# Kernel tuning notes

Hardware: AMD Instinct MI355X
Metric: run time of the kernel (lower is better)

Reference implementation:

```python
import jax, jax.numpy as jnp
import numpy as np

NUM_USERS = 60000
NUM_ITEMS = 40000
NUM_NODES = NUM_USERS + NUM_ITEMS
EMB = 64
HID = 32
N_EDGES = 1600000
BATCH = 16384


def setup_inputs() -> dict:
    key = jax.random.key(0)
    ks = jax.random.split(key, 16)
    def xavier(k, shape):
        fan_in, fan_out = shape[1], shape[0]
        lim = float(np.sqrt(6.0 / (fan_in + fan_out)))
        return jax.random.uniform(k, shape, jnp.float32, -lim, lim)
    return {
        "user_ids": jax.random.randint(ks[0], (BATCH,), 0, NUM_USERS),
        "item_ids": jax.random.randint(ks[1], (BATCH,), 0, NUM_ITEMS),
        "adj_rows": jax.random.randint(ks[2], (N_EDGES,), 0, NUM_NODES),
        "adj_cols": jax.random.randint(ks[3], (N_EDGES,), 0, NUM_NODES),
        "adj_vals": jax.random.uniform(ks[4], (N_EDGES,), jnp.float32),
        # embeddings (xavier_uniform, matching init_weights)
        "user_emb_w": xavier(ks[5], (NUM_USERS, EMB)),
        "item_emb_w": xavier(ks[6], (NUM_ITEMS, EMB)),
        # GC layer 1: 64 -> 32 ; GC layer 2: 32 -> 64
        "gc1_w": xavier(ks[7], (HID, EMB)),
        "gc1_b": jnp.zeros((HID,), jnp.float32),
        "gc2_w": xavier(ks[8], (EMB, HID)),
        "gc2_b": jnp.zeros((EMB,), jnp.float32),
        # predictor: Linear(2*EMB -> HID), ReLU, Linear(HID -> 1), Sigmoid
        "p1_w": xavier(ks[9], (HID, 2 * EMB)),
        "p1_b": jnp.zeros((HID,), jnp.float32),
        "p2_w": xavier(ks[10], (1, HID)),
        "p2_b": jnp.zeros((1,), jnp.float32),
    }


def _gc_layer(x, rows, cols, vals, w, b):
    # dense linear then spmm: out[i] = sum_e vals[e] * h[cols[e]] grouped by rows[e]
    h = x @ w.T + b                                # [N, out_dim]
    msg = vals[:, None] * h[cols]                  # [E, out_dim] gather (memory-bound)
    agg = jax.ops.segment_sum(msg, rows, num_segments=NUM_NODES)
    return jax.nn.relu(agg)                        # dropout in eval mode = identity


def reference(user_ids, item_ids, adj_rows, adj_cols, adj_vals,
              user_emb_w, item_emb_w, gc1_w, gc1_b, gc2_w, gc2_b,
              p1_w, p1_b, p2_w, p2_b):
    node_feat = jnp.concatenate([user_emb_w, item_emb_w], axis=0)  # [N, EMB]
    h = _gc_layer(node_feat, adj_rows, adj_cols, adj_vals, gc1_w, gc1_b)
    h = _gc_layer(h, adj_rows, adj_cols, adj_vals, gc2_w, gc2_b)
    final_user_emb = h[:NUM_USERS]
    final_item_emb = h[NUM_USERS:]
    bu = final_user_emb[user_ids]                  # [B, EMB]
    bi = final_item_emb[item_ids]                  # [B, EMB]
    z = jnp.concatenate([bu, bi], axis=1)          # [B, 2*EMB]
    z = jax.nn.relu(z @ p1_w.T + p1_b)             # [B, HID]
    scores = jax.nn.sigmoid(z @ p2_w.T + p2_b).squeeze(-1)  # [B]
    return (scores, final_user_emb, final_item_emb)
```

## Files before the change

kernel.cpp:

```cpp
#include <hip/hip_runtime.h>
#include <hip/hip_bf16.h>

#define NUM_USERS 60000
#define NUM_ITEMS 40000
#define NUM_NODES 100000
#define EMB 64
#define HID 32
#define N_EDGES 1600000
#define BATCH 16384

#define TILE 128
#define NBUCK 782
#define BLOCK_E 8192
#define NBLK_A 196
#define EPT 16
#define CAPB 3072

#define WS_CNTC   0
#define WS_BASEC  800
#define WS_CURC   1600
#define WS_ROFF   2400
#define WS_BINNED 102752
#define WS_H1     3302752
#define WS_G      6502752
#define WS_SUMV   9702752

__global__ __launch_bounds__(256) void k_hist_coarse(
    const int* __restrict__ rows, unsigned* __restrict__ cnt)
{
    __shared__ unsigned s[NBUCK];
    for (int i = threadIdx.x; i < NBUCK; i += 256) s[i] = 0u;
    __syncthreads();
    for (int e = blockIdx.x * 256 + threadIdx.x; e < N_EDGES; e += gridDim.x * 256)
        atomicAdd(&s[((unsigned)rows[e]) >> 7], 1u);
    __syncthreads();
    for (int i = threadIdx.x; i < NBUCK; i += 256)
        if (s[i]) atomicAdd(&cnt[i], s[i]);
}

__global__ __launch_bounds__(1024) void k_scanb(
    const unsigned* __restrict__ cnt,
    unsigned* __restrict__ base, unsigned* __restrict__ cursor)
{
    __shared__ unsigned s[1024];
    int t = threadIdx.x;
    unsigned v = (t < NBUCK) ? cnt[t] : 0u;
    s[t] = v;
    __syncthreads();
    #pragma unroll
    for (int ofs = 1; ofs < 1024; ofs <<= 1) {
        unsigned u = (t >= ofs) ? s[t - ofs] : 0u;
        __syncthreads();
        s[t] += u;
        __syncthreads();
    }
    if (t < NBUCK) {
        unsigned ex = s[t] - v;
        base[t] = ex;
        cursor[t] = ex;
    }
    if (t == 0) base[NBUCK] = N_EDGES;
}

__global__ __launch_bounds__(512) void k_partA(
    const int* __restrict__ rows, const int* __restrict__ cols,
    const float* __restrict__ vals,
    unsigned* __restrict__ cursor, uint2* __restrict__ binned)
{
    __shared__ unsigned cnt[NBUCK];
    __shared__ unsigned offs[NBUCK];
    __shared__ unsigned gbase[NBUCK];
    __shared__ unsigned scanbuf[1024];
    __shared__ uint2    staged[BLOCK_E];
    __shared__ unsigned dstarr[BLOCK_E];

    int t = threadIdx.x;
    for (int i = t; i < NBUCK; i += 512) cnt[i] = 0u;
    __syncthreads();

    unsigned eb = blockIdx.x * BLOCK_E;
    unsigned bb[EPT], rk[EPT];
    uint2    pr[EPT];
    #pragma unroll
    for (int i = 0; i < EPT; i++) {
        unsigned e = eb + (unsigned)(i * 512 + t);
        if (e < N_EDGES) {
            unsigned r = (unsigned)rows[e];
            bb[i] = r >> 7;
            pr[i] = make_uint2(((r & 127u) << 17) | (unsigned)cols[e],
                               __float_as_uint(vals[e]));
            rk[i] = atomicAdd(&cnt[bb[i]], 1u);
        } else {
            bb[i] = 0xFFFFFFFFu;
        }
    }
    __syncthreads();

    unsigned c0 = (t < NBUCK) ? cnt[t] : 0u;
    unsigned c1 = (t + 512 < NBUCK) ? cnt[t + 512] : 0u;
    scanbuf[t] = c0; scanbuf[t + 512] = c1;
    __syncthreads();
    #pragma unroll
    for (int ofs = 1; ofs < 1024; ofs <<= 1) {
        unsigned a0 = (t >= ofs) ? scanbuf[t - ofs] : 0u;
        unsigned a1 = (t + 512 >= ofs) ? scanbuf[t + 512 - ofs] : 0u;
        __syncthreads();
        scanbuf[t] += a0; scanbuf[t + 512] += a1;
        __syncthreads();
    }
    if (t < NBUCK) offs[t] = scanbuf[t] - c0;
    if (t + 512 < NBUCK) offs[t + 512] = scanbuf[t + 512] - c1;
    __syncthreads();

    for (int b = t; b < NBUCK; b += 512) {
        unsigned c = cnt[b];
        gbase[b] = c ? atomicAdd(&cursor[b], c) : 0u;
    }
    __syncthreads();

    #pragma unroll
    for (int i = 0; i < EPT; i++) {
        if (bb[i] != 0xFFFFFFFFu) {
            unsigned s = offs[bb[i]] + rk[i];
            staged[s] = pr[i];
            dstarr[s] = gbase[bb[i]] + rk[i];
        }
    }
    __syncthreads();

    unsigned total = (eb + BLOCK_E <= N_EDGES) ? (unsigned)BLOCK_E
                                               : (N_EDGES - eb);
    for (unsigned s = t; s < total; s += 512)
        binned[dstarr[s]] = staged[s];
}

__global__ __launch_bounds__(256) void k_partB(
    const unsigned* __restrict__ basec,
    uint2* __restrict__ binned, unsigned* __restrict__ roff)
{
    __shared__ uint2    st[CAPB];
    __shared__ uint2    ob[CAPB];
    __shared__ unsigned cnt[TILE];
    __shared__ unsigned sc[TILE];

    int t = threadIdx.x;
    int nb = blockIdx.x;
    unsigned gs = basec[nb];
    unsigned count = basec[nb + 1] - gs;
    if (count > CAPB) count = CAPB;

    for (int i = t; i < TILE; i += 256) cnt[i] = 0u;
    __syncthreads();

    unsigned rl_[CAPB / 256], rk_[CAPB / 256];
    uint2    pp_[CAPB / 256];
    #pragma unroll
    for (int it = 0; it < CAPB / 256; it++) {
        unsigned s = (unsigned)t + it * 256u;
        if (s < count) {
            uint2 p = binned[gs + s];
            unsigned rl = p.x >> 17;
            pp_[it] = p;
            rl_[it] = rl;
            rk_[it] = atomicAdd(&cnt[rl], 1u);
            st[s] = p;
        } else {
            rl_[it] = 0xFFFFFFFFu;
        }
    }
    __syncthreads();

    unsigned c = (t < TILE) ? cnt[t] : 0u;
    if (t < TILE) sc[t] = c;
    __syncthreads();
    #pragma unroll
    for (int ofs = 1; ofs < TILE; ofs <<= 1) {
        unsigned a = 0u;
        if (t < TILE && t >= ofs) a = sc[t - ofs];
        __syncthreads();
        if (t < TILE) sc[t] += a;
        __syncthreads();
    }
    __shared__ unsigned offs[TILE];
    if (t < TILE) offs[t] = sc[t] - c;
    __syncthreads();

    for (int i = t; i <= TILE; i += 256) {
        int n = nb * TILE + i;
        if (n <= NUM_NODES)
            roff[n] = gs + ((i < TILE) ? offs[i] : count);
    }

    #pragma unroll
    for (int it = 0; it < CAPB / 256; it++) {
        if (rl_[it] != 0xFFFFFFFFu)
            ob[offs[rl_[it]] + rk_[it]] = pp_[it];
    }
    __syncthreads();
    for (unsigned s = (unsigned)t; s < count; s += 256)
        binned[gs + s] = ob[s];
}

template<bool RELU, bool SUMV>
__global__ __launch_bounds__(256) void k_agg32(
    const unsigned* __restrict__ roff, const uint2* __restrict__ binned,
    const float* __restrict__ H, float* __restrict__ out,
    float* __restrict__ sumv_out)
{
    int wave = threadIdx.x >> 6;
    int lane = threadIdx.x & 63;
    int n = blockIdx.x * 4 + wave;
    if (n >= NUM_NODES) return;
    int g = lane >> 3;
    int q = lane & 7;
    unsigned s = roff[n], e = roff[n + 1];
    float4 acc = make_float4(0.f, 0.f, 0.f, 0.f);
    float sv = 0.f;
    for (unsigned k = s + (unsigned)g; k < e; k += 8u) {
        uint2 p = binned[k];
        unsigned col = p.x & 0x1FFFFu;
        float v = __uint_as_float(p.y);
        float4 h = reinterpret_cast<const float4*>(H + (size_t)col * HID)[q];
        acc.x = fmaf(v, h.x, acc.x);
        acc.y = fmaf(v, h.y, acc.y);
        acc.z = fmaf(v, h.z, acc.z);
        acc.w = fmaf(v, h.w, acc.w);
        if (SUMV) sv += v;
    }
    #pragma unroll
    for (int m = 8; m < 64; m <<= 1) {
        acc.x += __shfl_xor(acc.x, m);
        acc.y += __shfl_xor(acc.y, m);
        acc.z += __shfl_xor(acc.z, m);
        acc.w += __shfl_xor(acc.w, m);
        if (SUMV) sv += __shfl_xor(sv, m);
    }
    if (g == 0) {
        if (RELU) {
            acc.x = fmaxf(acc.x, 0.f); acc.y = fmaxf(acc.y, 0.f);
            acc.z = fmaxf(acc.z, 0.f); acc.w = fmaxf(acc.w, 0.f);
        }
        reinterpret_cast<float4*>(out + (size_t)n * HID)[q] = acc;
        if (SUMV && q == 0) sumv_out[n] = sv;
    }
}

__global__ __launch_bounds__(256) void k_linear1(
    const float* __restrict__ ue, const float* __restrict__ ie,
    const float* __restrict__ w, const float* __restrict__ b,
    float* __restrict__ out)
{
    __shared__ float ws[HID * EMB];
    __shared__ float bs[HID];
    for (int i = threadIdx.x; i < HID * EMB; i += 256) ws[i] = w[i];
    if (threadIdx.x < HID) bs[threadIdx.x] = b[threadIdx.x];
    __syncthreads();

    int n = blockIdx.x * 256 + threadIdx.x;
    if (n >= NUM_NODES) return;
    const float* row = (n < NUM_USERS) ? ue + (size_t)n * EMB
                                       : ie + (size_t)(n - NUM_USERS) * EMB;
    float x[EMB];
    #pragma unroll
    for (int k4 = 0; k4 < EMB / 4; k4++) {
        float4 v = reinterpret_cast<const float4*>(row)[k4];
        x[4*k4+0] = v.x; x[4*k4+1] = v.y; x[4*k4+2] = v.z; x[4*k4+3] = v.w;
    }
    const float4* ws4 = reinterpret_cast<const float4*>(ws);
    float acc[HID];
    #pragma unroll
    for (int j = 0; j < HID; j++) {
        float a = bs[j];
        #pragma unroll
        for (int k4 = 0; k4 < EMB / 4; k4++) {
            float4 wv = ws4[j * (EMB/4) + k4];
            a = fmaf(wv.x, x[4*k4+0], a);
            a = fmaf(wv.y, x[4*k4+1], a);
            a = fmaf(wv.z, x[4*k4+2], a);
            a = fmaf(wv.w, x[4*k4+3], a);
        }
        acc[j] = a;
    }
    float4* o4 = reinterpret_cast<float4*>(out + (size_t)n * HID);
    #pragma unroll
    for (int j4 = 0; j4 < HID / 4; j4++)
        o4[j4] = make_float4(acc[4*j4], acc[4*j4+1], acc[4*j4+2], acc[4*j4+3]);
}

__global__ __launch_bounds__(256) void k_linear2_post(
    const float* __restrict__ G, const float* __restrict__ sumv,
    const float* __restrict__ w, const float* __restrict__ b,
    float* __restrict__ out)
{
    __shared__ float ws[EMB * HID];
    __shared__ float bs[EMB];
    for (int i = threadIdx.x; i < EMB * HID; i += 256) ws[i] = w[i];
    if (threadIdx.x < EMB) bs[threadIdx.x] = b[threadIdx.x];
    __syncthreads();

    int n = blockIdx.x * 256 + threadIdx.x;
    if (n >= NUM_NODES) return;
    const float* row = G + (size_t)n * HID;
    float sv = sumv[n];
    float x[HID];
    #pragma unroll
    for (int k4 = 0; k4 < HID / 4; k4++) {
        float4 v = reinterpret_cast<const float4*>(row)[k4];
        x[4*k4+0] = v.x; x[4*k4+1] = v.y; x[4*k4+2] = v.z; x[4*k4+3] = v.w;
    }
    const float4* ws4 = reinterpret_cast<const float4*>(ws);
    float acc[EMB];
    #pragma unroll
    for (int j = 0; j < EMB; j++) {
        float a = sv * bs[j];
        #pragma unroll
        for (int k4 = 0; k4 < HID / 4; k4++) {
            float4 wv = ws4[j * (HID/4) + k4];
            a = fmaf(wv.x, x[4*k4+0], a);
            a = fmaf(wv.y, x[4*k4+1], a);
            a = fmaf(wv.z, x[4*k4+2], a);
            a = fmaf(wv.w, x[4*k4+3], a);
        }
        acc[j] = fmaxf(a, 0.f);
    }
    float4* o4 = reinterpret_cast<float4*>(out + (size_t)n * EMB);
    #pragma unroll
    for (int j4 = 0; j4 < EMB / 4; j4++)
        o4[j4] = make_float4(acc[4*j4], acc[4*j4+1], acc[4*j4+2], acc[4*j4+3]);
}

__global__ __launch_bounds__(256) void k_mlp(
    const int* __restrict__ uids, const int* __restrict__ iids,
    const float* __restrict__ uemb, const float* __restrict__ iemb,
    const float* __restrict__ p1w, const float* __restrict__ p1b,
    const float* __restrict__ p2w, const float* __restrict__ p2b,
    float* __restrict__ scores)
{
    __shared__ float w1t[2 * EMB * HID];
    __shared__ float zt[8][2 * EMB];
    __shared__ float b1s[HID];
    __shared__ float w2s[HID];

    for (int i = threadIdx.x; i < HID * 2 * EMB; i += 256) {
        int j = i >> 7;
        int k = i & 127;
        int k4 = k >> 2, c = k & 3;
        w1t[k4 * 128 + j * 4 + c] = p1w[i];
    }
    if (threadIdx.x < HID) {
        b1s[threadIdx.x] = p1b[threadIdx.x];
        w2s[threadIdx.x] = p2w[threadIdx.x];
    }
    __syncthreads();

    int lg = threadIdx.x >> 5;
    int j  = threadIdx.x & 31;
    int s  = blockIdx.x * 8 + lg;

    {
        int u  = uids[s];
        int it = iids[s];
        const float* bu = uemb + (size_t)u * EMB;
        const float* bi = iemb + (size_t)it * EMB;
        float* zs = zt[lg];
        zs[j]      = bu[j];
        zs[32 + j] = bu[32 + j];
        zs[64 + j] = bi[j];
        zs[96 + j] = bi[32 + j];
    }
    __syncthreads();

    const float*  zs = zt[lg];
    const float4* w4 = reinterpret_cast<const float4*>(w1t);
    const float4* z4 = reinterpret_cast<const float4*>(zs);
    float a = b1s[j];
    #pragma unroll
    for (int k4 = 0; k4 < 32; k4++) {
        float4 wv = w4[k4 * 32 + j];
        float4 zv = z4[k4];
        a = fmaf(wv.x, zv.x, a);
        a = fmaf(wv.y, zv.y, a);
        a = fmaf(wv.z, zv.z, a);
        a = fmaf(wv.w, zv.w, a);
    }
    a = fmaxf(a, 0.f);
    float part = a * w2s[j];
    #pragma unroll
    for (int m = 16; m >= 1; m >>= 1) part += __shfl_xor(part, m);
    if (j == 0) scores[s] = 1.f / (1.f + expf(-(part + p2b[0])));
}

extern "C" void kernel_launch(void* const* d_in, const int* in_sizes, int n_in,
                              void* d_out, int out_size, void* d_ws, size_t ws_size,
                              hipStream_t stream)
{
    const int*   user_ids = (const int*)  d_in[0];
    const int*   item_ids = (const int*)  d_in[1];
    const int*   adj_rows = (const int*)  d_in[2];
    const int*   adj_cols = (const int*)  d_in[3];
    const float* adj_vals = (const float*)d_in[4];
    const float* user_emb = (const float*)d_in[5];
    const float* item_emb = (const float*)d_in[6];
    const float* gc1_w    = (const float*)d_in[7];
    const float* gc1_b    = (const float*)d_in[8];
    const float* gc2_w    = (const float*)d_in[9];
    const float* gc2_b    = (const float*)d_in[10];
    const float* p1_w     = (const float*)d_in[11];
    const float* p1_b     = (const float*)d_in[12];
    const float* p2_w     = (const float*)d_in[13];
    const float* p2_b     = (const float*)d_in[14];

    float* out     = (float*)d_out;
    float* scores  = out;
    float* emb_out = out + BATCH;

    unsigned* ws_u   = (unsigned*)d_ws;
    unsigned* cntc   = ws_u + WS_CNTC;
    unsigned* basec  = ws_u + WS_BASEC;
    unsigned* curc   = ws_u + WS_CURC;
    unsigned* roff   = ws_u + WS_ROFF;
    uint2*    binned = (uint2*)(ws_u + WS_BINNED);
    float*    H1     = (float*)(ws_u + WS_H1);
    float*    G      = (float*)(ws_u + WS_G);
    float*    SUMV   = (float*)(ws_u + WS_SUMV);
    float*    A1     = emb_out;

    hipMemsetAsync(cntc, 0, NBUCK * sizeof(unsigned), stream);
    k_hist_coarse<<<512, 256, 0, stream>>>(adj_rows, cntc);
    k_scanb<<<1, 1024, 0, stream>>>(cntc, basec, curc);
    k_partA<<<NBLK_A, 512, 0, stream>>>(adj_rows, adj_cols, adj_vals,
                                        curc, binned);
    k_partB<<<NBUCK, 256, 0, stream>>>(basec, binned, roff);

    k_linear1<<<(NUM_NODES + 255) / 256, 256, 0, stream>>>(
        user_emb, item_emb, gc1_w, gc1_b, H1);
    k_agg32<true, false><<<NUM_NODES / 4, 256, 0, stream>>>(
        roff, binned, H1, A1, nullptr);

    k_agg32<false, true><<<NUM_NODES / 4, 256, 0, stream>>>(
        roff, binned, A1, G, SUMV);
    k_linear2_post<<<(NUM_NODES + 255) / 256, 256, 0, stream>>>(
        G, SUMV, gc2_w, gc2_b, emb_out);

    k_mlp<<<BATCH / 8, 256, 0, stream>>>(
        user_ids, item_ids, emb_out, emb_out + (size_t)NUM_USERS * EMB,
        p1_w, p1_b, p2_w, p2_b, scores);
}
```

Before: 292.3 us.

## Replace histogram+scan with fixed-capacity buckets and unroll aggregation gather loop

Removes the coarse histogram pass, the memset and the single-block scan. Each bucket now gets a fixed slot of CAPB entries, so partition A writes through cursors starting at bucket*CAPB, and partition B reads its count from the final cursor and records a per-bucket end offset. The aggregation kernel reads that end offset for the last node of each tile and processes two edges per iteration to expose more memory-level parallelism. Partition A also uses smaller blocks (more blocks with fewer edges each). Risks: a bucket holding more than CAPB edges would overflow its slot, the binned buffer is larger, and the stale staging write in partition B is dropped.

```diff
diff --git a/kernel.cpp b/kernel.cpp
--- a/kernel.cpp
+++ b/kernel.cpp
@@ -11,55 +11,24 @@
 
 #define TILE 128
 #define NBUCK 782
-#define BLOCK_E 8192
-#define NBLK_A 196
-#define EPT 16
 #define CAPB 3072
-
-#define WS_CNTC   0
-#define WS_BASEC  800
-#define WS_CURC   1600
-#define WS_ROFF   2400
-#define WS_BINNED 102752
-#define WS_H1     3302752
-#define WS_G      6502752
-#define WS_SUMV   9702752
-
-__global__ __launch_bounds__(256) void k_hist_coarse(
-    const int* __restrict__ rows, unsigned* __restrict__ cnt)
-{
-    __shared__ unsigned s[NBUCK];
-    for (int i = threadIdx.x; i < NBUCK; i += 256) s[i] = 0u;
-    __syncthreads();
-    for (int e = blockIdx.x * 256 + threadIdx.x; e < N_EDGES; e += gridDim.x * 256)
-        atomicAdd(&s[((unsigned)rows[e]) >> 7], 1u);
-    __syncthreads();
-    for (int i = threadIdx.x; i < NBUCK; i += 256)
-        if (s[i]) atomicAdd(&cnt[i], s[i]);
-}
-
-__global__ __launch_bounds__(1024) void k_scanb(
-    const unsigned* __restrict__ cnt,
-    unsigned* __restrict__ base, unsigned* __restrict__ cursor)
-{
-    __shared__ unsigned s[1024];
+#define BLOCK_E 4096
+#define NBLK_A 391
+#define EPT 8
+#define EPT_B (CAPB / 256)
+
+#define WS_CUR    0
+#define WS_BEND   800
+#define WS_ROFF   1600
+#define WS_BINNED 101952
+#define WS_H1     4906560
+#define WS_G      8106560
+#define WS_SUMV   11306560
+
+__global__ __launch_bounds__(1024) void k_initcur(unsigned* __restrict__ cur)
+{
     int t = threadIdx.x;
-    unsigned v = (t < NBUCK) ? cnt[t] : 0u;
-    s[t] = v;
-    __syncthreads();
-    #pragma unroll
-    for (int ofs = 1; ofs < 1024; ofs <<= 1) {
-        unsigned u = (t >= ofs) ? s[t - ofs] : 0u;
-        __syncthreads();
-        s[t] += u;
-        __syncthreads();
-    }
-    if (t < NBUCK) {
-        unsigned ex = s[t] - v;
-        base[t] = ex;
-        cursor[t] = ex;
-    }
-    if (t == 0) base[NBUCK] = N_EDGES;
+    if (t < NBUCK) cur[t] = (unsigned)t * CAPB;
 }
 
 __global__ __launch_bounds__(512) void k_partA(
@@ -135,27 +104,28 @@
 }
 
 __global__ __launch_bounds__(256) void k_partB(
-    const unsigned* __restrict__ basec,
-    uint2* __restrict__ binned, unsigned* __restrict__ roff)
-{
-    __shared__ uint2    st[CAPB];
+    const unsigned* __restrict__ cursor,
+    uint2* __restrict__ binned,
+    unsigned* __restrict__ roff, unsigned* __restrict__ bend)
+{
     __shared__ uint2    ob[CAPB];
     __shared__ unsigned cnt[TILE];
     __shared__ unsigned sc[TILE];
+    __shared__ unsigned offs[TILE];
 
     int t = threadIdx.x;
     int nb = blockIdx.x;
-    unsigned gs = basec[nb];
-    unsigned count = basec[nb + 1] - gs;
+    unsigned gs = (unsigned)nb * CAPB;
+    unsigned count = cursor[nb] - gs;
     if (count > CAPB) count = CAPB;
 
     for (int i = t; i < TILE; i += 256) cnt[i] = 0u;
     __syncthreads();
 
-    unsigned rl_[CAPB / 256], rk_[CAPB / 256];
-    uint2    pp_[CAPB / 256];
-    #pragma unroll
-    for (int it = 0; it < CAPB / 256; it++) {
+    unsigned rl_[EPT_B], rk_[EPT_B];
+    uint2    pp_[EPT_B];
+    #pragma unroll
+    for (int it = 0; it < EPT_B; it++) {
         unsigned s = (unsigned)t + it * 256u;
         if (s < count) {
             uint2 p = binned[gs + s];
@@ -163,7 +133,6 @@
             pp_[it] = p;
             rl_[it] = rl;
             rk_[it] = atomicAdd(&cnt[rl], 1u);
-            st[s] = p;
         } else {
             rl_[it] = 0xFFFFFFFFu;
         }
@@ -181,18 +150,17 @@
         if (t < TILE) sc[t] += a;
         __syncthreads();
     }
-    __shared__ unsigned offs[TILE];
     if (t < TILE) offs[t] = sc[t] - c;
     __syncthreads();
 
-    for (int i = t; i <= TILE; i += 256) {
+    for (int i = t; i < TILE; i += 256) {
         int n = nb * TILE + i;
-        if (n <= NUM_NODES)
-            roff[n] = gs + ((i < TILE) ? offs[i] : count);
-    }
-
-    #pragma unroll
-    for (int it = 0; it < CAPB / 256; it++) {
+        if (n <= NUM_NODES) roff[n] = gs + offs[i];
+    }
+    if (t == 0) bend[nb] = gs + count;
+
+    #pragma unroll
+    for (int it = 0; it < EPT_B; it++) {
         if (rl_[it] != 0xFFFFFFFFu)
             ob[offs[rl_[it]] + rk_[it]] = pp_[it];
     }
@@ -203,7 +171,8 @@
 
 template<bool RELU, bool SUMV>
 __global__ __launch_bounds__(256) void k_agg32(
-    const unsigned* __restrict__ roff, const uint2* __restrict__ binned,
+    const unsigned* __restrict__ roff, const unsigned* __restrict__ bend,
+    const uint2* __restrict__ binned,
     const float* __restrict__ H, float* __restrict__ out,
     float* __restrict__ sumv_out)
 {
@@ -213,18 +182,30 @@
     if (n >= NUM_NODES) return;
     int g = lane >> 3;
     int q = lane & 7;
-    unsigned s = roff[n], e = roff[n + 1];
+    unsigned s = roff[n];
+    unsigned e = ((n & 127) == 127) ? bend[n >> 7] : roff[n + 1];
     float4 acc = make_float4(0.f, 0.f, 0.f, 0.f);
     float sv = 0.f;
-    for (unsigned k = s + (unsigned)g; k < e; k += 8u) {
+    unsigned k = s + (unsigned)g;
+    for (; k + 8u < e; k += 16u) {
+        uint2 pa = binned[k];
+        uint2 pb = binned[k + 8u];
+        float va = __uint_as_float(pa.y);
+        float vb = __uint_as_float(pb.y);
+        float4 ha = reinterpret_cast<const float4*>(H + (size_t)(pa.x & 0x1FFFFu) * HID)[q];
+        float4 hb = reinterpret_cast<const float4*>(H + (size_t)(pb.x & 0x1FFFFu) * HID)[q];
+        acc.x = fmaf(va, ha.x, acc.x); acc.y = fmaf(va, ha.y, acc.y);
+        acc.z = fmaf(va, ha.z, acc.z); acc.w = fmaf(va, ha.w, acc.w);
+        acc.x = fmaf(vb, hb.x, acc.x); acc.y = fmaf(vb, hb.y, acc.y);
+        acc.z = fmaf(vb, hb.z, acc.z); acc.w = fmaf(vb, hb.w, acc.w);
+        if (SUMV) sv += va + vb;
+    }
+    if (k < e) {
         uint2 p = binned[k];
-        unsigned col = p.x & 0x1FFFFu;
         float v = __uint_as_float(p.y);
-        float4 h = reinterpret_cast<const float4*>(H + (size_t)col * HID)[q];
-        acc.x = fmaf(v, h.x, acc.x);
-        acc.y = fmaf(v, h.y, acc.y);
-        acc.z = fmaf(v, h.z, acc.z);
-        acc.w = fmaf(v, h.w, acc.w);
+        float4 h = reinterpret_cast<const float4*>(H + (size_t)(p.x & 0x1FFFFu) * HID)[q];
+        acc.x = fmaf(v, h.x, acc.x); acc.y = fmaf(v, h.y, acc.y);
+        acc.z = fmaf(v, h.z, acc.z); acc.w = fmaf(v, h.w, acc.w);
         if (SUMV) sv += v;
     }
     #pragma unroll
@@ -415,9 +396,8 @@
     float* emb_out = out + BATCH;
 
     unsigned* ws_u   = (unsigned*)d_ws;
-    unsigned* cntc   = ws_u + WS_CNTC;
-    unsigned* basec  = ws_u + WS_BASEC;
-    unsigned* curc   = ws_u + WS_CURC;
+    unsigned* cur    = ws_u + WS_CUR;
+    unsigned* bend   = ws_u + WS_BEND;
     unsigned* roff   = ws_u + WS_ROFF;
     uint2*    binned = (uint2*)(ws_u + WS_BINNED);
     float*    H1     = (float*)(ws_u + WS_H1);
@@ -425,20 +405,18 @@
     float*    SUMV   = (float*)(ws_u + WS_SUMV);
     float*    A1     = emb_out;
 
-    hipMemsetAsync(cntc, 0, NBUCK * sizeof(unsigned), stream);
-    k_hist_coarse<<<512, 256, 0, stream>>>(adj_rows, cntc);
-    k_scanb<<<1, 1024, 0, stream>>>(cntc, basec, curc);
+    k_initcur<<<1, 1024, 0, stream>>>(cur);
     k_partA<<<NBLK_A, 512, 0, stream>>>(adj_rows, adj_cols, adj_vals,
-                                        curc, binned);
-    k_partB<<<NBUCK, 256, 0, stream>>>(basec, binned, roff);
+                                        cur, binned);
+    k_partB<<<NBUCK, 256, 0, stream>>>(cur, binned, roff, bend);
 
     k_linear1<<<(NUM_NODES + 255) / 256, 256, 0, stream>>>(
         user_emb, item_emb, gc1_w, gc1_b, H1);
     k_agg32<true, false><<<NUM_NODES / 4, 256, 0, stream>>>(
-        roff, binned, H1, A1, nullptr);
+        roff, bend, binned, H1, A1, nullptr);
 
     k_agg32<false, true><<<NUM_NODES / 4, 256, 0, stream>>>(
-        roff, binned, A1, G, SUMV);
+        roff, bend, binned, A1, G, SUMV);
     k_linear2_post<<<(NUM_NODES + 255) / 256, 256, 0, stream>>>(
         G, SUMV, gc2_w, gc2_b, emb_out);
 
```

Result: faster. 267.7 us (-8.4%).
